# Kernel tuning notes

Hardware: AMD Instinct MI355X
Metric: run time of the kernel (lower is better)

Reference implementation:

```python
import jax, jax.numpy as jnp
import numpy as np

N_NODES = 100000
N_EDGES = 1600000
IN_F = 128
OUT_F = 64


def setup_inputs() -> dict:
    key = jax.random.key(0)
    k1, k2, k3, k4, k5, k6 = jax.random.split(key, 6)
    stdv = 1.0 / np.sqrt(OUT_F)
    return {
        "input": jax.random.normal(k1, (N_NODES, IN_F), dtype=jnp.float32),
        "weights": jax.random.uniform(k2, (IN_F, OUT_F), minval=-stdv, maxval=stdv, dtype=jnp.float32),
        "bias": jax.random.uniform(k3, (OUT_F,), minval=-stdv, maxval=stdv, dtype=jnp.float32),
        "adj_vals": jax.random.uniform(k4, (N_EDGES,), dtype=jnp.float32),
        "adj_rows": jax.random.randint(k5, (N_EDGES,), 0, N_NODES, dtype=jnp.int32),
        "adj_cols": jax.random.randint(k6, (N_EDGES,), 0, N_NODES, dtype=jnp.int32),
    }


def reference(input, weights, bias, adj_vals, adj_rows, adj_cols):
    # Dense transform: support = input @ W   -> [N, out_features]
    support = jnp.matmul(input, weights)
    # Sparse adjacency matmul (COO SpMM): out[r] += v * support[c]
    msgs = adj_vals[:, None] * support[adj_cols]          # [E, out_features]
    output = jax.ops.segment_sum(msgs, adj_rows, num_segments=N_NODES)
    # Fused bias epilogue
    return output + bias
```

## Files before the change

### kernel.cpp

```cpp
#include <hip/hip_runtime.h>
#include <hip/hip_bf16.h>

#define N_NODES 100000
#define IN_F 128
#define OUT_F 64
#define BROWS 64
#define NB 1563
#define BIN_TILE 4096
#define CSB_CAP 2048

typedef __attribute__((ext_vector_type(8))) short bf16x8;
typedef __attribute__((ext_vector_type(4))) float f32x4;

__device__ __forceinline__ unsigned short f2bf(float x) {
    unsigned u = __float_as_uint(x);
    u += 0x7FFFu + ((u >> 16) & 1u);
    return (unsigned short)(u >> 16);
}
__device__ __forceinline__ float bf2f(unsigned short s) {
    return __uint_as_float(((unsigned)s) << 16);
}

__global__ __launch_bounds__(256) void wt_kernel(
    const float* __restrict__ W, unsigned short* __restrict__ Wt)
{
    int i = blockIdx.x * 256 + threadIdx.x;
    if (i < IN_F * OUT_F) {
        int c = i >> 7, k = i & 127;
        Wt[i] = f2bf(W[k * OUT_F + c]);
    }
}

__global__ __launch_bounds__(256) void gemm_mfma(
    const float* __restrict__ in, const unsigned short* __restrict__ Wt,
    unsigned short* __restrict__ support)
{
    const int t    = threadIdx.x;
    const int lane = t & 63;
    const int rw   = t >> 6;
    const long row0 = (long)blockIdx.x * 64 + rw * 16;

    const int lr = lane & 15;
    const int lk = lane >> 4;

    long arow = row0 + lr;
    if (arow >= N_NODES) arow = N_NODES - 1;
    const float* Ap = in + arow * IN_F + lk * 8;
    const unsigned short* Wp = Wt + lk * 8;

    f32x4 acc0 = {0.f, 0.f, 0.f, 0.f};
    f32x4 acc1 = {0.f, 0.f, 0.f, 0.f};
    f32x4 acc2 = {0.f, 0.f, 0.f, 0.f};
    f32x4 acc3 = {0.f, 0.f, 0.f, 0.f};

    #pragma unroll
    for (int ks = 0; ks < 4; ++ks) {
        const float4 a01 = *(const float4*)(Ap + ks * 32);
        const float4 a23 = *(const float4*)(Ap + ks * 32 + 4);
        bf16x8 af;
        af[0] = (short)f2bf(a01.x); af[1] = (short)f2bf(a01.y);
        af[2] = (short)f2bf(a01.z); af[3] = (short)f2bf(a01.w);
        af[4] = (short)f2bf(a23.x); af[5] = (short)f2bf(a23.y);
        af[6] = (short)f2bf(a23.z); af[7] = (short)f2bf(a23.w);

        const int koff = ks * 32;
        bf16x8 b0 = *(const bf16x8*)(Wp + (0 * 16 + lr) * IN_F + koff);
        bf16x8 b1 = *(const bf16x8*)(Wp + (1 * 16 + lr) * IN_F + koff);
        bf16x8 b2 = *(const bf16x8*)(Wp + (2 * 16 + lr) * IN_F + koff);
        bf16x8 b3 = *(const bf16x8*)(Wp + (3 * 16 + lr) * IN_F + koff);

        acc0 = __builtin_amdgcn_mfma_f32_16x16x32_bf16(af, b0, acc0, 0, 0, 0);
        acc1 = __builtin_amdgcn_mfma_f32_16x16x32_bf16(af, b1, acc1, 0, 0, 0);
        acc2 = __builtin_amdgcn_mfma_f32_16x16x32_bf16(af, b2, acc2, 0, 0, 0);
        acc3 = __builtin_amdgcn_mfma_f32_16x16x32_bf16(af, b3, acc3, 0, 0, 0);
    }

    #pragma unroll
    for (int r = 0; r < 4; ++r) {
        const long orow = row0 + lk * 4 + r;
        if (orow < N_NODES) {
            unsigned short* o = support + orow * OUT_F;
            o[ 0 + lr] = f2bf(acc0[r]);
            o[16 + lr] = f2bf(acc1[r]);
            o[32 + lr] = f2bf(acc2[r]);
            o[48 + lr] = f2bf(acc3[r]);
        }
    }
}

__global__ __launch_bounds__(256) void count_kernel(
    const int* __restrict__ rows, int* __restrict__ cnt, int nE)
{
    __shared__ int hist[NB];
    const int t = threadIdx.x;
    for (int i = t; i < NB; i += 256) hist[i] = 0;
    __syncthreads();

    for (int e = blockIdx.x * 256 + t; e < nE; e += gridDim.x * 256)
        atomicAdd(&hist[rows[e] >> 6], 1);
    __syncthreads();

    for (int i = t; i < NB; i += 256) {
        int h = hist[i];
        if (h) atomicAdd(&cnt[i], h);
    }
}

__global__ __launch_bounds__(256) void scan_kernel(
    const int* __restrict__ cnt, int* __restrict__ base,
    int* __restrict__ cursor, int nE)
{
    __shared__ int lds[256];
    const int t = threadIdx.x;
    const int i0 = t * 8;
    int c[8];
    int tot = 0;
    #pragma unroll
    for (int k = 0; k < 8; ++k) {
        c[k] = (i0 + k < NB) ? cnt[i0 + k] : 0;
        tot += c[k];
    }

    lds[t] = tot;
    __syncthreads();
    int sum = tot;
    #pragma unroll
    for (int off = 1; off < 256; off <<= 1) {
        int y = (t >= off) ? lds[t - off] : 0;
        __syncthreads();
        sum += y;
        lds[t] = sum;
        __syncthreads();
    }
    int run = sum - tot;

    #pragma unroll
    for (int k = 0; k < 8; ++k) {
        if (i0 + k < NB) { base[i0 + k] = run; cursor[i0 + k] = run; }
        run += c[k];
    }
    if (t == 0) base[NB] = nE;
}

__global__ __launch_bounds__(256) void bin_kernel(
    const int* __restrict__ rows, const int* __restrict__ cols,
    const float* __restrict__ vals, int* __restrict__ cursor,
    uint2* __restrict__ binned, int nE)
{
    __shared__ int hist[NB];
    __shared__ int lbase[NB];
    const int t  = threadIdx.x;
    const int tb = blockIdx.x * BIN_TILE;

    for (int i = t; i < NB; i += 256) hist[i] = 0;
    __syncthreads();

    int myr[16], myrank[16];
    #pragma unroll
    for (int i = 0; i < 16; ++i) {
        int e = tb + i * 256 + t;
        if (e < nE) {
            int r = rows[e];
            myr[i] = r;
            myrank[i] = atomicAdd(&hist[r >> 6], 1);
        } else myr[i] = -1;
    }
    __syncthreads();

    for (int i = t; i < NB; i += 256) {
        int h = hist[i];
        lbase[i] = h ? atomicAdd(&cursor[i], h) : 0;
    }
    __syncthreads();

    #pragma unroll
    for (int i = 0; i < 16; ++i) {
        int e = tb + i * 256 + t;
        if (e < nE) {
            int r = myr[i];
            unsigned pack = ((unsigned)(r & (BROWS - 1)) << 17) | (unsigned)cols[e];
            binned[lbase[r >> 6] + myrank[i]] =
                make_uint2(pack, __float_as_uint(vals[e]));
        }
    }
}

__global__ __launch_bounds__(1024, 2) void csr_spmm(
    const int* __restrict__ base, const uint2* __restrict__ binned,
    const unsigned short* __restrict__ support, const float* __restrict__ bias,
    float* __restrict__ out)
{
    __shared__ uint2 stage[CSB_CAP];
    __shared__ uint2 sorted[CSB_CAP];
    __shared__ int rh[BROWS], rs[BROWS + 1], rc[BROWS];
    const int t = threadIdx.x;
    const int b = blockIdx.x;
    const int s = base[b], e = base[b + 1];
    const int n = e - s;
    const int wid  = t >> 6;
    const int lane = t & 63;
    const int row0 = b * BROWS;

    if (t < BROWS) rh[t] = 0;
    __syncthreads();

    if (n <= CSB_CAP) {
        for (int i = t; i < n; i += 1024) {
            uint2 p = binned[s + i];
            stage[i] = p;
            atomicAdd(&rh[p.x >> 17], 1);
        }
        __syncthreads();
        if (t < BROWS) {
            int v = rh[t];
            int inc = v;
            #pragma unroll
            for (int off = 1; off < BROWS; off <<= 1) {
                int y = __shfl_up(inc, off, 64);
                if (t >= off) inc += y;
            }
            rs[t] = inc - v;
            rc[t] = inc - v;
            if (t == BROWS - 1) rs[BROWS] = inc;
        }
        __syncthreads();
        for (int i = t; i < n; i += 1024) {
            uint2 p = stage[i];
            int pos = atomicAdd(&rc[p.x >> 17], 1);
            sorted[pos] = p;
        }
        __syncthreads();

        #pragma unroll
        for (int q = 0; q < 4; ++q) {
            const int rr = wid * 4 + q;
            const int r  = row0 + rr;
            if (r >= N_NODES) break;
            float acc = bias[lane];
            int j  = rs[rr];
            const int je = rs[rr + 1];
            for (; j + 7 < je; j += 8) {
                uint2 q0 = sorted[j + 0];
                uint2 q1 = sorted[j + 1];
                uint2 q2 = sorted[j + 2];
                uint2 q3 = sorted[j + 3];
                uint2 q4 = sorted[j + 4];
                uint2 q5 = sorted[j + 5];
                uint2 q6 = sorted[j + 6];
                uint2 q7 = sorted[j + 7];
                float g0 = bf2f(support[((size_t)(q0.x & 131071u) << 6) + lane]);
                float g1 = bf2f(support[((size_t)(q1.x & 131071u) << 6) + lane]);
                float g2 = bf2f(support[((size_t)(q2.x & 131071u) << 6) + lane]);
                float g3 = bf2f(support[((size_t)(q3.x & 131071u) << 6) + lane]);
                float g4 = bf2f(support[((size_t)(q4.x & 131071u) << 6) + lane]);
                float g5 = bf2f(support[((size_t)(q5.x & 131071u) << 6) + lane]);
                float g6 = bf2f(support[((size_t)(q6.x & 131071u) << 6) + lane]);
                float g7 = bf2f(support[((size_t)(q7.x & 131071u) << 6) + lane]);
                acc = fmaf(__uint_as_float(q0.y), g0, acc);
                acc = fmaf(__uint_as_float(q1.y), g1, acc);
                acc = fmaf(__uint_as_float(q2.y), g2, acc);
                acc = fmaf(__uint_as_float(q3.y), g3, acc);
                acc = fmaf(__uint_as_float(q4.y), g4, acc);
                acc = fmaf(__uint_as_float(q5.y), g5, acc);
                acc = fmaf(__uint_as_float(q6.y), g6, acc);
                acc = fmaf(__uint_as_float(q7.y), g7, acc);
            }
            for (; j < je; ++j) {
                uint2 p = sorted[j];
                acc = fmaf(__uint_as_float(p.y),
                           bf2f(support[((size_t)(p.x & 131071u) << 6) + lane]),
                           acc);
            }
            out[(size_t)r * OUT_F + lane] = acc;
        }
    } else {
        #pragma unroll
        for (int q = 0; q < 4; ++q) {
            const int rr = wid * 4 + q;
            const int r  = row0 + rr;
            if (r >= N_NODES) break;
            float acc = bias[lane];
            for (int j = s; j < e; ++j) {
                uint2 p = binned[j];
                if ((int)(p.x >> 17) == rr)
                    acc = fmaf(__uint_as_float(p.y),
                               bf2f(support[((size_t)(p.x & 131071u) << 6) + lane]),
                               acc);
            }
            out[(size_t)r * OUT_F + lane] = acc;
        }
    }
}

__global__ __launch_bounds__(256) void gemm_valu(
    const float* __restrict__ in, const float* __restrict__ W,
    unsigned short* __restrict__ support)
{
    __shared__ float Alds[64 * IN_F];
    const int t = threadIdx.x;
    const long row0 = (long)blockIdx.x * 64;
    #pragma unroll
    for (int i = 0; i < 8; ++i) {
        int fi = t + i * 256;
        int r  = fi >> 5;
        int c4 = (fi & 31) << 2;
        float4 v = make_float4(0.f, 0.f, 0.f, 0.f);
        if (row0 + r < N_NODES)
            v = *(const float4*)(in + (row0 + r) * IN_F + c4);
        *(float4*)(Alds + r * IN_F + c4) = v;
    }
    __syncthreads();
    const int lane = t & 63;
    const int c0   = __builtin_amdgcn_readfirstlane((t >> 6) << 4);
    const float* __restrict__ Wp = W + c0;
    float acc[16];
    #pragma unroll
    for (int i = 0; i < 16; ++i) acc[i] = 0.f;
    const float* Ar = Alds + lane * IN_F;
    for (int k = 0; k < IN_F; ++k) {
        const float a = Ar[k];
        const float4 w0 = *(const float4*)(Wp + k * OUT_F + 0);
        const float4 w1 = *(const float4*)(Wp + k * OUT_F + 4);
        const float4 w2 = *(const float4*)(Wp + k * OUT_F + 8);
        const float4 w3 = *(const float4*)(Wp + k * OUT_F + 12);
        acc[0]  = fmaf(a, w0.x, acc[0]);  acc[1]  = fmaf(a, w0.y, acc[1]);
        acc[2]  = fmaf(a, w0.z, acc[2]);  acc[3]  = fmaf(a, w0.w, acc[3]);
        acc[4]  = fmaf(a, w1.x, acc[4]);  acc[5]  = fmaf(a, w1.y, acc[5]);
        acc[6]  = fmaf(a, w1.z, acc[6]);  acc[7]  = fmaf(a, w1.w, acc[7]);
        acc[8]  = fmaf(a, w2.x, acc[8]);  acc[9]  = fmaf(a, w2.y, acc[9]);
        acc[10] = fmaf(a, w2.z, acc[10]); acc[11] = fmaf(a, w2.w, acc[11]);
        acc[12] = fmaf(a, w3.x, acc[12]); acc[13] = fmaf(a, w3.y, acc[13]);
        acc[14] = fmaf(a, w3.z, acc[14]); acc[15] = fmaf(a, w3.w, acc[15]);
    }
    const long orow = row0 + lane;
    if (orow < N_NODES) {
        unsigned short* o = support + orow * OUT_F + c0;
        #pragma unroll
        for (int i = 0; i < 16; ++i) o[i] = f2bf(acc[i]);
    }
}

__global__ __launch_bounds__(256) void bias_init_kernel(
    float* __restrict__ out, const float* __restrict__ bias, int total4)
{
    const float4* b4 = (const float4*)bias;
    float4* o4 = (float4*)out;
    int i = blockIdx.x * blockDim.x + threadIdx.x;
    int stride = gridDim.x * blockDim.x;
    for (; i < total4; i += stride)
        o4[i] = b4[i & 15];
}

__global__ __launch_bounds__(256) void scatter_kernel(
    const float* __restrict__ vals, const int* __restrict__ rows,
    const int* __restrict__ cols, const unsigned short* __restrict__ support,
    float* __restrict__ out, int nE)
{
    const int e = blockIdx.x * 4 + (threadIdx.x >> 6);
    if (e >= nE) return;
    const int f = threadIdx.x & 63;
    const float m = vals[e] * bf2f(support[(size_t)cols[e] * OUT_F + f]);
    atomicAdd(&out[(size_t)rows[e] * OUT_F + f], m);
}

extern "C" void kernel_launch(void* const* d_in, const int* in_sizes, int n_in,
                              void* d_out, int out_size, void* d_ws, size_t ws_size,
                              hipStream_t stream) {
    const float* input    = (const float*)d_in[0];
    const float* weights  = (const float*)d_in[1];
    const float* bias     = (const float*)d_in[2];
    const float* adj_vals = (const float*)d_in[3];
    const int*   adj_rows = (const int*)d_in[4];
    const int*   adj_cols = (const int*)d_in[5];
    const int nE = in_sizes[3];

    float* out = (float*)d_out;
    const int gemmBlocks = (N_NODES + 63) / 64;
    const int binBlocks  = (nE + BIN_TILE - 1) / BIN_TILE;

    char* ws = (char*)d_ws;
    const size_t off_support = 0;
    const size_t off_wt      = 12800000;
    const size_t off_base    = off_wt + 16384;
    const size_t off_cursor  = off_base + 6400;
    const size_t off_binned  = off_cursor + 6400;
    const size_t required    = off_binned + (size_t)nE * 8;

    unsigned short* support = (unsigned short*)(ws + off_support);
    unsigned short* Wt      = (unsigned short*)(ws + off_wt);
    int*   bbase   = (int*)  (ws + off_base);
    int*   cursor  = (int*)  (ws + off_cursor);
    uint2* binned  = (uint2*)(ws + off_binned);

    if (ws_size >= required) {
        hipMemsetAsync(cursor, 0, NB * sizeof(int), stream);
        hipLaunchKernelGGL(count_kernel, dim3(256), dim3(256), 0, stream,
                           adj_rows, cursor, nE);
        hipLaunchKernelGGL(scan_kernel, dim3(1), dim3(256), 0, stream,
                           cursor, bbase, cursor, nE);
        hipLaunchKernelGGL(wt_kernel, dim3(32), dim3(256), 0, stream,
                           weights, Wt);
        hipLaunchKernelGGL(gemm_mfma, dim3(gemmBlocks), dim3(256), 0, stream,
                           input, Wt, support);
        hipLaunchKernelGGL(bin_kernel, dim3(binBlocks), dim3(256), 0, stream,
                           adj_rows, adj_cols, adj_vals, cursor, binned, nE);
        hipLaunchKernelGGL(csr_spmm, dim3(NB), dim3(1024), 0, stream,
                           bbase, binned, support, bias, out);
    } else {
        hipLaunchKernelGGL(gemm_valu, dim3(gemmBlocks), dim3(256), 0, stream,
                           input, weights, support);
        hipLaunchKernelGGL(bias_init_kernel, dim3(2048), dim3(256), 0, stream,
                           out, bias, N_NODES * OUT_F / 4);
        hipLaunchKernelGGL(scatter_kernel, dim3((nE + 3) / 4), dim3(256),
                           0, stream, adj_vals, adj_rows, adj_cols, support,
                           out, nE);
    }
}
```

Measured before the change: 134.9 us.

## Replace count+scan binning with fixed-capacity buckets plus overflow list; stage GEMM stores via LDS

Removes the count_kernel pass over all row indices and the single-block scan by giving each 64-row bucket a fixed slot region of BCAP entries. Edges beyond capacity go to a global overflow list that a small atomic fixup kernel adds after the SpMM. The GEMM epilogue now stages bf16 results in LDS so global stores are coalesced 8-byte writes. The trade-off is a larger workspace, and the overflow path uses float atomics in an order that is not deterministic. Average bucket load is about 1024 edges, so the 1280 cap should rarely overflow.

```diff
diff --git a/kernel.cpp b/kernel.cpp
--- a/kernel.cpp
+++ b/kernel.cpp
@@ -7,7 +7,9 @@
 #define BROWS 64
 #define NB 1563
 #define BIN_TILE 4096
-#define CSB_CAP 2048
+#define BCAP 1280
+#define OVCAP 131072
+#define CSB_CAP 1280
 
 typedef __attribute__((ext_vector_type(8))) short bf16x8;
 typedef __attribute__((ext_vector_type(4))) float f32x4;
@@ -35,10 +37,12 @@
     const float* __restrict__ in, const unsigned short* __restrict__ Wt,
     unsigned short* __restrict__ support)
 {
+    __shared__ unsigned short Dl[64 * 68];
     const int t    = threadIdx.x;
     const int lane = t & 63;
     const int rw   = t >> 6;
-    const long row0 = (long)blockIdx.x * 64 + rw * 16;
+    const long rowB = (long)blockIdx.x * 64;
+    const long row0 = rowB + rw * 16;
 
     const int lr = lane & 15;
     const int lk = lane >> 4;
@@ -75,76 +79,34 @@
         acc3 = __builtin_amdgcn_mfma_f32_16x16x32_bf16(af, b3, acc3, 0, 0, 0);
     }
 
+    const int lrow = rw * 16 + lk * 4;
     #pragma unroll
     for (int r = 0; r < 4; ++r) {
-        const long orow = row0 + lk * 4 + r;
+        unsigned short* dst = Dl + (lrow + r) * 68;
+        dst[ 0 + lr] = f2bf(acc0[r]);
+        dst[16 + lr] = f2bf(acc1[r]);
+        dst[32 + lr] = f2bf(acc2[r]);
+        dst[48 + lr] = f2bf(acc3[r]);
+    }
+    __syncthreads();
+
+    #pragma unroll
+    for (int i = 0; i < 4; ++i) {
+        const int idx = t + i * 256;
+        const int row = idx >> 4;
+        const int c2  = idx & 15;
+        const long orow = rowB + row;
         if (orow < N_NODES) {
-            unsigned short* o = support + orow * OUT_F;
-            o[ 0 + lr] = f2bf(acc0[r]);
-            o[16 + lr] = f2bf(acc1[r]);
-            o[32 + lr] = f2bf(acc2[r]);
-            o[48 + lr] = f2bf(acc3[r]);
-        }
-    }
-}
-
-__global__ __launch_bounds__(256) void count_kernel(
-    const int* __restrict__ rows, int* __restrict__ cnt, int nE)
-{
-    __shared__ int hist[NB];
-    const int t = threadIdx.x;
-    for (int i = t; i < NB; i += 256) hist[i] = 0;
-    __syncthreads();
-
-    for (int e = blockIdx.x * 256 + t; e < nE; e += gridDim.x * 256)
-        atomicAdd(&hist[rows[e] >> 6], 1);
-    __syncthreads();
-
-    for (int i = t; i < NB; i += 256) {
-        int h = hist[i];
-        if (h) atomicAdd(&cnt[i], h);
-    }
-}
-
-__global__ __launch_bounds__(256) void scan_kernel(
-    const int* __restrict__ cnt, int* __restrict__ base,
-    int* __restrict__ cursor, int nE)
-{
-    __shared__ int lds[256];
-    const int t = threadIdx.x;
-    const int i0 = t * 8;
-    int c[8];
-    int tot = 0;
-    #pragma unroll
-    for (int k = 0; k < 8; ++k) {
-        c[k] = (i0 + k < NB) ? cnt[i0 + k] : 0;
-        tot += c[k];
-    }
-
-    lds[t] = tot;
-    __syncthreads();
-    int sum = tot;
-    #pragma unroll
-    for (int off = 1; off < 256; off <<= 1) {
-        int y = (t >= off) ? lds[t - off] : 0;
-        __syncthreads();
-        sum += y;
-        lds[t] = sum;
-        __syncthreads();
-    }
-    int run = sum - tot;
-
-    #pragma unroll
-    for (int k = 0; k < 8; ++k) {
-        if (i0 + k < NB) { base[i0 + k] = run; cursor[i0 + k] = run; }
-        run += c[k];
-    }
-    if (t == 0) base[NB] = nE;
+            const uint2 v = *(const uint2*)(Dl + row * 68 + c2 * 4);
+            *(uint2*)(support + orow * OUT_F + c2 * 4) = v;
+        }
+    }
 }
 
 __global__ __launch_bounds__(256) void bin_kernel(
     const int* __restrict__ rows, const int* __restrict__ cols,
     const float* __restrict__ vals, int* __restrict__ cursor,
+    int* __restrict__ ovCount, uint4* __restrict__ ovList,
     uint2* __restrict__ binned, int nE)
 {
     __shared__ int hist[NB];
@@ -177,16 +139,26 @@
     for (int i = 0; i < 16; ++i) {
         int e = tb + i * 256 + t;
         if (e < nE) {
-            int r = myr[i];
-            unsigned pack = ((unsigned)(r & (BROWS - 1)) << 17) | (unsigned)cols[e];
-            binned[lbase[r >> 6] + myrank[i]] =
-                make_uint2(pack, __float_as_uint(vals[e]));
+            const int r = myr[i];
+            const int b = r >> 6;
+            const int off = lbase[b] + myrank[i];
+            if (off < BCAP) {
+                unsigned pack = ((unsigned)(r & (BROWS - 1)) << 17)
+                              | (unsigned)cols[e];
+                binned[(size_t)b * BCAP + off] =
+                    make_uint2(pack, __float_as_uint(vals[e]));
+            } else {
+                int op = atomicAdd(ovCount, 1);
+                if (op < OVCAP)
+                    ovList[op] = make_uint4((unsigned)r, (unsigned)cols[e],
+                                            __float_as_uint(vals[e]), 0u);
+            }
         }
     }
 }
 
 __global__ __launch_bounds__(1024, 2) void csr_spmm(
-    const int* __restrict__ base, const uint2* __restrict__ binned,
+    const int* __restrict__ cursor, const uint2* __restrict__ binned,
     const unsigned short* __restrict__ support, const float* __restrict__ bias,
     float* __restrict__ out)
 {
@@ -195,8 +167,8 @@
     __shared__ int rh[BROWS], rs[BROWS + 1], rc[BROWS];
     const int t = threadIdx.x;
     const int b = blockIdx.x;
-    const int s = base[b], e = base[b + 1];
-    const int n = e - s;
+    const size_t s = (size_t)b * BCAP;
+    const int n = min(cursor[b], BCAP);
     const int wid  = t >> 6;
     const int lane = t & 63;
     const int row0 = b * BROWS;
@@ -204,91 +176,87 @@
     if (t < BROWS) rh[t] = 0;
     __syncthreads();
 
-    if (n <= CSB_CAP) {
-        for (int i = t; i < n; i += 1024) {
-            uint2 p = binned[s + i];
-            stage[i] = p;
-            atomicAdd(&rh[p.x >> 17], 1);
-        }
-        __syncthreads();
-        if (t < BROWS) {
-            int v = rh[t];
-            int inc = v;
-            #pragma unroll
-            for (int off = 1; off < BROWS; off <<= 1) {
-                int y = __shfl_up(inc, off, 64);
-                if (t >= off) inc += y;
-            }
-            rs[t] = inc - v;
-            rc[t] = inc - v;
-            if (t == BROWS - 1) rs[BROWS] = inc;
-        }
-        __syncthreads();
-        for (int i = t; i < n; i += 1024) {
-            uint2 p = stage[i];
-            int pos = atomicAdd(&rc[p.x >> 17], 1);
-            sorted[pos] = p;
-        }
-        __syncthreads();
-
+    for (int i = t; i < n; i += 1024) {
+        uint2 p = binned[s + i];
+        stage[i] = p;
+        atomicAdd(&rh[p.x >> 17], 1);
+    }
+    __syncthreads();
+    if (t < BROWS) {
+        int v = rh[t];
+        int inc = v;
         #pragma unroll
-        for (int q = 0; q < 4; ++q) {
-            const int rr = wid * 4 + q;
-            const int r  = row0 + rr;
-            if (r >= N_NODES) break;
-            float acc = bias[lane];
-            int j  = rs[rr];
-            const int je = rs[rr + 1];
-            for (; j + 7 < je; j += 8) {
-                uint2 q0 = sorted[j + 0];
-                uint2 q1 = sorted[j + 1];
-                uint2 q2 = sorted[j + 2];
-                uint2 q3 = sorted[j + 3];
-                uint2 q4 = sorted[j + 4];
-                uint2 q5 = sorted[j + 5];
-                uint2 q6 = sorted[j + 6];
-                uint2 q7 = sorted[j + 7];
-                float g0 = bf2f(support[((size_t)(q0.x & 131071u) << 6) + lane]);
-                float g1 = bf2f(support[((size_t)(q1.x & 131071u) << 6) + lane]);
-                float g2 = bf2f(support[((size_t)(q2.x & 131071u) << 6) + lane]);
-                float g3 = bf2f(support[((size_t)(q3.x & 131071u) << 6) + lane]);
-                float g4 = bf2f(support[((size_t)(q4.x & 131071u) << 6) + lane]);
-                float g5 = bf2f(support[((size_t)(q5.x & 131071u) << 6) + lane]);
-                float g6 = bf2f(support[((size_t)(q6.x & 131071u) << 6) + lane]);
-                float g7 = bf2f(support[((size_t)(q7.x & 131071u) << 6) + lane]);
-                acc = fmaf(__uint_as_float(q0.y), g0, acc);
-                acc = fmaf(__uint_as_float(q1.y), g1, acc);
-                acc = fmaf(__uint_as_float(q2.y), g2, acc);
-                acc = fmaf(__uint_as_float(q3.y), g3, acc);
-                acc = fmaf(__uint_as_float(q4.y), g4, acc);
-                acc = fmaf(__uint_as_float(q5.y), g5, acc);
-                acc = fmaf(__uint_as_float(q6.y), g6, acc);
-                acc = fmaf(__uint_as_float(q7.y), g7, acc);
-            }
-            for (; j < je; ++j) {
-                uint2 p = sorted[j];
-                acc = fmaf(__uint_as_float(p.y),
-                           bf2f(support[((size_t)(p.x & 131071u) << 6) + lane]),
-                           acc);
-            }
-            out[(size_t)r * OUT_F + lane] = acc;
-        }
-    } else {
-        #pragma unroll
-        for (int q = 0; q < 4; ++q) {
-            const int rr = wid * 4 + q;
-            const int r  = row0 + rr;
-            if (r >= N_NODES) break;
-            float acc = bias[lane];
-            for (int j = s; j < e; ++j) {
-                uint2 p = binned[j];
-                if ((int)(p.x >> 17) == rr)
-                    acc = fmaf(__uint_as_float(p.y),
-                               bf2f(support[((size_t)(p.x & 131071u) << 6) + lane]),
-                               acc);
-            }
-            out[(size_t)r * OUT_F + lane] = acc;
-        }
+        for (int off = 1; off < BROWS; off <<= 1) {
+            int y = __shfl_up(inc, off, 64);
+            if (t >= off) inc += y;
+        }
+        rs[t] = inc - v;
+        rc[t] = inc - v;
+        if (t == BROWS - 1) rs[BROWS] = inc;
+    }
+    __syncthreads();
+    for (int i = t; i < n; i += 1024) {
+        uint2 p = stage[i];
+        int pos = atomicAdd(&rc[p.x >> 17], 1);
+        sorted[pos] = p;
+    }
+    __syncthreads();
+
+    #pragma unroll
+    for (int q = 0; q < 4; ++q) {
+        const int rr = wid * 4 + q;
+        const int r  = row0 + rr;
+        if (r >= N_NODES) break;
+        float acc = bias[lane];
+        int j  = rs[rr];
+        const int je = rs[rr + 1];
+        for (; j + 7 < je; j += 8) {
+            uint2 q0 = sorted[j + 0];
+            uint2 q1 = sorted[j + 1];
+            uint2 q2 = sorted[j + 2];
+            uint2 q3 = sorted[j + 3];
+            uint2 q4 = sorted[j + 4];
+            uint2 q5 = sorted[j + 5];
+            uint2 q6 = sorted[j + 6];
+            uint2 q7 = sorted[j + 7];
+            float g0 = bf2f(support[((size_t)(q0.x & 131071u) << 6) + lane]);
+            float g1 = bf2f(support[((size_t)(q1.x & 131071u) << 6) + lane]);
+            float g2 = bf2f(support[((size_t)(q2.x & 131071u) << 6) + lane]);
+            float g3 = bf2f(support[((size_t)(q3.x & 131071u) << 6) + lane]);
+            float g4 = bf2f(support[((size_t)(q4.x & 131071u) << 6) + lane]);
+            float g5 = bf2f(support[((size_t)(q5.x & 131071u) << 6) + lane]);
+            float g6 = bf2f(support[((size_t)(q6.x & 131071u) << 6) + lane]);
+            float g7 = bf2f(support[((size_t)(q7.x & 131071u) << 6) + lane]);
+            acc = fmaf(__uint_as_float(q0.y), g0, acc);
+            acc = fmaf(__uint_as_float(q1.y), g1, acc);
+            acc = fmaf(__uint_as_float(q2.y), g2, acc);
+            acc = fmaf(__uint_as_float(q3.y), g3, acc);
+            acc = fmaf(__uint_as_float(q4.y), g4, acc);
+            acc = fmaf(__uint_as_float(q5.y), g5, acc);
+            acc = fmaf(__uint_as_float(q6.y), g6, acc);
+            acc = fmaf(__uint_as_float(q7.y), g7, acc);
+        }
+        for (; j < je; ++j) {
+            uint2 p = sorted[j];
+            acc = fmaf(__uint_as_float(p.y),
+                       bf2f(support[((size_t)(p.x & 131071u) << 6) + lane]),
+                       acc);
+        }
+        out[(size_t)r * OUT_F + lane] = acc;
+    }
+}
+
+__global__ __launch_bounds__(256) void ovfix_kernel(
+    const int* __restrict__ ovCount, const uint4* __restrict__ ovList,
+    const unsigned short* __restrict__ support, float* __restrict__ out)
+{
+    const int n = min(*ovCount, OVCAP);
+    const int lane = threadIdx.x & 63;
+    for (int e = blockIdx.x * 4 + (threadIdx.x >> 6); e < n; e += 32 * 4) {
+        const uint4 p = ovList[e];
+        const float m = __uint_as_float(p.z) *
+                        bf2f(support[((size_t)p.y << 6) + lane]);
+        atomicAdd(&out[((size_t)p.x << 6) + lane], m);
     }
 }
 
@@ -381,31 +349,31 @@
     char* ws = (char*)d_ws;
     const size_t off_support = 0;
     const size_t off_wt      = 12800000;
-    const size_t off_base    = off_wt + 16384;
-    const size_t off_cursor  = off_base + 6400;
-    const size_t off_binned  = off_cursor + 6400;
-    const size_t required    = off_binned + (size_t)nE * 8;
+    const size_t off_cursor  = off_wt + 16384;
+    const size_t off_binned  = off_cursor + 6272;
+    const size_t off_ovlist  = off_binned + (size_t)NB * BCAP * 8;
+    const size_t required    = off_ovlist + (size_t)OVCAP * 16;
 
     unsigned short* support = (unsigned short*)(ws + off_support);
     unsigned short* Wt      = (unsigned short*)(ws + off_wt);
-    int*   bbase   = (int*)  (ws + off_base);
     int*   cursor  = (int*)  (ws + off_cursor);
     uint2* binned  = (uint2*)(ws + off_binned);
+    uint4* ovList  = (uint4*)(ws + off_ovlist);
+    int*   ovCount = cursor + NB;
 
     if (ws_size >= required) {
-        hipMemsetAsync(cursor, 0, NB * sizeof(int), stream);
-        hipLaunchKernelGGL(count_kernel, dim3(256), dim3(256), 0, stream,
-                           adj_rows, cursor, nE);
-        hipLaunchKernelGGL(scan_kernel, dim3(1), dim3(256), 0, stream,
-                           cursor, bbase, cursor, nE);
+        hipMemsetAsync(cursor, 0, (NB + 1) * sizeof(int), stream);
         hipLaunchKernelGGL(wt_kernel, dim3(32), dim3(256), 0, stream,
                            weights, Wt);
         hipLaunchKernelGGL(gemm_mfma, dim3(gemmBlocks), dim3(256), 0, stream,
                            input, Wt, support);
         hipLaunchKernelGGL(bin_kernel, dim3(binBlocks), dim3(256), 0, stream,
-                           adj_rows, adj_cols, adj_vals, cursor, binned, nE);
+                           adj_rows, adj_cols, adj_vals, cursor,
+                           ovCount, ovList, binned, nE);
         hipLaunchKernelGGL(csr_spmm, dim3(NB), dim3(1024), 0, stream,
-                           bbase, binned, support, bias, out);
+                           cursor, binned, support, bias, out);
+        hipLaunchKernelGGL(ovfix_kernel, dim3(32), dim3(256), 0, stream,
+                           ovCount, ovList, support, out);
     } else {
         hipLaunchKernelGGL(gemm_valu, dim3(gemmBlocks), dim3(256), 0, stream,
                            input, weights, support);
```

After: 117.3 us. 13.0% less time.
